# Optimization experiments

Hardware: AMD Instinct MI355X
Metric: run time of the kernel (lower is better)

The kernel has to match this reference:

```python
import jax, jax.numpy as jnp
import numpy as np

N = 50000      # nodes
E = 400000     # edges
D = 256        # args.dimensions
H1 = 32        # hidden1 (per-head)
HEADS = 4      # gat_heads
H2 = 64        # hidden2
DEC = 512      # decoder1
B = 4096       # number of entity index pairs
NEG = 0.2      # PyG GATConv leaky_relu negative slope


def setup_inputs() -> dict:
    key = jax.random.key(0)
    ks = jax.random.split(key, 24)
    s = lambda k, shape, fan: jax.random.normal(k, shape, jnp.float32) * (1.0 / np.sqrt(fan))
    return {
        "x_o": jax.random.normal(ks[0], (N, D), jnp.float32),
        "x_a": jax.random.normal(ks[1], (N, D), jnp.float32),
        "edge_index": jax.random.randint(ks[2], (2, E), 0, N, jnp.int32),
        "idx": jax.random.randint(ks[3], (2, B), 0, N, jnp.int32),
        # GATConv 1: in D -> H1 per head, HEADS heads, concat
        "W1": s(ks[4], (D, HEADS * H1), D),
        "a_src1": s(ks[5], (HEADS, H1), H1),
        "a_dst1": s(ks[6], (HEADS, H1), H1),
        "b1": jnp.zeros((HEADS * H1,), jnp.float32),
        "p1": jnp.full((HEADS * H1,), 0.25, jnp.float32),   # PReLU weight
        # GATConv 2: HEADS*H1 -> H2, 1 head, no concat
        "W2": s(ks[7], (HEADS * H1, H2), HEADS * H1),
        "a_src2": s(ks[8], (1, H2), H2),
        "a_dst2": s(ks[9], (1, H2), H2),
        "b2": jnp.zeros((H2,), jnp.float32),
        "p2": jnp.full((H2,), 0.25, jnp.float32),
        # mlp1
        "mlp_W": s(ks[10], (H2, H2), H2),
        "mlp_b": jnp.zeros((H2,), jnp.float32),
        # Discriminator bilinear (out=1)
        "disc_W": s(ks[11], (H2, H2), H2),
        "disc_b": jnp.zeros((), jnp.float32),
        # adversarial_logits linear (fixed, deterministic stand-in)
        "adv_W": s(ks[12], (H2, H2), H2),
        "adv_b": jnp.zeros((H2,), jnp.float32),
        # fusion decoder (stand-in for build_fusion_decoder): MLP with 2 heads
        "f_W1": s(ks[13], (2 * H2, DEC), 2 * H2),
        "f_b1": jnp.zeros((DEC,), jnp.float32),
        "f_W2": s(ks[14], (DEC, 2), DEC),
        "f_b2": jnp.zeros((2,), jnp.float32),
        "f_W3": s(ks[15], (DEC, 2), DEC),
        "f_b3": jnp.zeros((2,), jnp.float32),
    }


def prelu(x, w):
    return jnp.where(x >= 0, x, w * x)


def gat_conv(x, src, dst, W, a_src, a_dst, b, heads, out_dim, concat):
    # PyG GATConv (eval): per-head linear, edge attention, dst-segment softmax, scatter-sum.
    n = x.shape[0]
    h = (x @ W).reshape(n, heads, out_dim)                  # [N, H, F]
    a_s = (h * a_src[None]).sum(-1)                         # [N, H]
    a_d = (h * a_dst[None]).sum(-1)                         # [N, H]
    e = jax.nn.leaky_relu(a_s[src] + a_d[dst], NEG)         # [E', H]
    e_max = jax.ops.segment_max(e, dst, num_segments=n)
    w = jnp.exp(e - e_max[dst])
    denom = jax.ops.segment_sum(w, dst, num_segments=n)
    alpha = w / (denom[dst] + 1e-16)                        # [E', H]
    out = jax.ops.segment_sum(h[src] * alpha[..., None], dst, num_segments=n)  # [N, H, F]
    out = out.reshape(n, heads * out_dim) if concat else out.mean(1)
    return out + b


def encode(x, src, dst, W1, a_src1, a_dst1, b1, p1, W2, a_src2, a_dst2, b2, p2):
    x1 = prelu(gat_conv(x, src, dst, W1, a_src1, a_dst1, b1, HEADS, H1, True), p1)
    x2 = gat_conv(x1, src, dst, W2, a_src2, a_dst2, b2, 1, H2, False)
    return prelu(x2, p2)


def discriminate(c, h_pl, h_mi, disc_W, disc_b):
    # nn.Bilinear(n_h, n_h, 1) against broadcast summary c
    Wc = disc_W @ c                                          # [H2]
    sc_1 = h_pl @ Wc + disc_b                                # [N]
    sc_2 = h_mi @ Wc + disc_b                                # [N]
    return jnp.stack([sc_1, sc_2], axis=1)                   # [N, 2]


def reference(x_o, x_a, edge_index, idx,
              W1, a_src1, a_dst1, b1, p1,
              W2, a_src2, a_dst2, b2, p2,
              mlp_W, mlp_b, disc_W, disc_b, adv_W, adv_b,
              f_W1, f_b1, f_W2, f_b2, f_W3, f_b3):
    n = x_o.shape[0]
    loops = jnp.arange(n, dtype=edge_index.dtype)            # PyG add_self_loops=True
    src = jnp.concatenate([edge_index[0], loops])
    dst = jnp.concatenate([edge_index[1], loops])

    x2_o = encode(x_o, src, dst, W1, a_src1, a_dst1, b1, p1, W2, a_src2, a_dst2, b2, p2)
    x2_o_a = encode(x_a, src, dst, W1, a_src1, a_dst1, b1, p1, W2, a_src2, a_dst2, b2, p2)

    h_os = jax.nn.sigmoid(x2_o.mean(0)) @ mlp_W + mlp_b      # AvgReadout -> sigmoid -> mlp1
    h_os_a = jax.nn.sigmoid(x2_o_a.mean(0)) @ mlp_W + mlp_b

    ret_os = discriminate(h_os, x2_o, x2_o_a, disc_W, disc_b)
    ret_os_a = discriminate(h_os_a, x2_o_a, x2_o, disc_W, disc_b)

    # entities (task_type 'other' branch)
    e1 = x2_o[idx[0]]
    e2 = x2_o[idx[1]]
    fh = jax.nn.relu(jnp.concatenate([e1, e2], axis=-1) @ f_W1 + f_b1)
    log = fh @ f_W2 + f_b2
    log1 = fh @ f_W3 + f_b3

    sc_1 = (x2_o @ adv_W + adv_b).sum(1)[None, :]            # [1, N]
    sc_2 = (x2_o_a @ adv_W + adv_b).sum(1)[None, :]
    logits = jnp.concatenate([sc_1, sc_2], axis=1)           # [1, 2N]

    return (log, ret_os, ret_os_a, x2_o, logits, log1)
```

## Files before the change

### kernel.cpp

```cpp
#include <hip/hip_runtime.h>
#include <hip/hip_bf16.h>
#include <math.h>

constexpr int NN   = 50000;
constexpr int N2   = 2*NN;
constexpr int EE   = 400000;
constexpr int DIN  = 256;
constexpr int M1   = 128;
constexpr int H1N  = 4;
constexpr int M2   = 64;
constexpr int BP   = 4096;
constexpr int DEC  = 512;
constexpr float SLOPE = 0.2f;

constexpr int O_LOG    = 0;
constexpr int O_RETOS  = 8192;
constexpr int O_RETOSA = 108192;
constexpr int O_X2     = 208192;
constexpr int O_LOGITS = 3408192;
constexpr int O_LOG1   = 3508192;

constexpr int SCAN_NB = (NN + 1023) / 1024;

typedef __attribute__((ext_vector_type(8))) short short8;
typedef __attribute__((ext_vector_type(4))) float f32x4;

__device__ __forceinline__ short f2bs(float v){
    __hip_bfloat16 h = __float2bfloat16(v);
    unsigned short u; __builtin_memcpy(&u, &h, 2);
    return (short)u;
}
__device__ __forceinline__ float lrelu(float e){ return (e >= 0.f) ? e : SLOPE*e; }

__global__ void hist_dst(const int* __restrict__ edst, int* __restrict__ cnt){
    int i = blockIdx.x*blockDim.x + threadIdx.x;
    if (i < EE) atomicAdd(&cnt[edst[i]], 1);
}

__global__ __launch_bounds__(1024) void scan_blk(const int* __restrict__ cnt,
                                                 int* __restrict__ rowex,
                                                 int* __restrict__ bsum){
    __shared__ int wsum[16];
    const int t = threadIdx.x;
    const int idx = blockIdx.x*1024 + t;
    const int lane = t & 63, wid = t >> 6;
    int v = (idx < NN) ? cnt[idx] : 0;
    int s = v;
    #pragma unroll
    for (int o = 1; o < 64; o <<= 1){
        int u = __shfl_up(s, o, 64);
        if (lane >= o) s += u;
    }
    if (lane == 63) wsum[wid] = s;
    __syncthreads();
    if (wid == 0){
        int ws = (lane < 16) ? wsum[lane] : 0;
        #pragma unroll
        for (int o = 1; o < 16; o <<= 1){
            int u = __shfl_up(ws, o, 64);
            if (lane >= o) ws += u;
        }
        if (lane < 16) wsum[lane] = ws;
    }
    __syncthreads();
    int base = (wid > 0) ? wsum[wid-1] : 0;
    int incl = base + s;
    if (idx < NN) rowex[idx] = incl - v;
    if (t == 1023) bsum[blockIdx.x] = incl;
}

__global__ void scan_bsum(int* __restrict__ bsum, int nb){
    const int lane = threadIdx.x;
    int v = (lane < nb) ? bsum[lane] : 0;
    int s = v;
    #pragma unroll
    for (int o = 1; o < 64; o <<= 1){
        int u = __shfl_up(s, o, 64);
        if (lane >= o) s += u;
    }
    if (lane < nb) bsum[lane] = s - v;
}

__global__ void scan_fix(int* __restrict__ row, const int* __restrict__ bsum,
                         int* __restrict__ cursor){
    int idx = blockIdx.x*blockDim.x + threadIdx.x;
    if (idx < NN){
        int r = row[idx] + bsum[idx >> 10];
        row[idx] = r;
        cursor[idx] = r;
    }
    if (idx == 0) row[NN] = EE;
}

__global__ void fill_csr(const int* __restrict__ esrc, const int* __restrict__ edst,
                         int* __restrict__ cursor, int* __restrict__ adj){
    int i = blockIdx.x*blockDim.x + threadIdx.x;
    if (i >= EE) return;
    int d = edst[i];
    int slot = atomicAdd(&cursor[d], 1);
    adj[slot] = esrc[i];
}

__device__ __forceinline__ void pack_one(const float* __restrict__ W,
                                         __hip_bfloat16* __restrict__ Wpk,
                                         int i, int M){
    int k = i / M, c = i - k*M;
    int kb = k >> 5, r = k & 31, quad = r >> 3, j = r & 7;
    int ct = c >> 4, ln = quad*16 + (c & 15);
    int CT = M >> 4;
    size_t dst = (((size_t)kb*CT + ct)*64 + ln)*8 + j;
    Wpk[dst] = __float2bfloat16(W[i]);
}

__global__ void pack_all(const float* __restrict__ W1, const float* __restrict__ W2,
                         const float* __restrict__ fW1,
                         __hip_bfloat16* __restrict__ Wpk1,
                         __hip_bfloat16* __restrict__ Wpk2,
                         __hip_bfloat16* __restrict__ Wpkf){
    constexpr int S1 = DIN*M1;
    constexpr int S2 = S1 + M1*M2;
    constexpr int S3 = S2 + M1*DEC;
    int i = blockIdx.x*blockDim.x + threadIdx.x;
    if (i < S1)       pack_one(W1,  Wpk1, i,      M1);
    else if (i < S2)  pack_one(W2,  Wpk2, i - S1, M2);
    else if (i < S3)  pack_one(fW1, Wpkf, i - S2, DEC);
}

template<int K, int M, int HEADS_T, bool AF32>
__global__ __launch_bounds__(256) void gemm_attn(
        const void* __restrict__ X0, const void* __restrict__ X1,
        const __hip_bfloat16* __restrict__ Wpk,
        const float* __restrict__ asrc, const float* __restrict__ adst,
        __hip_bfloat16* __restrict__ Hb,
        float* __restrict__ AS, float* __restrict__ AD){
    constexpr int CT = M/16;
    constexpr int KB = K/32;
    constexpr int CPH = CT/HEADS_T;
    const int wave = (blockIdx.x*256 + threadIdx.x) >> 6;
    const int lane = threadIdx.x & 63;
    const int n0 = wave*16;
    if (n0 >= N2) return;
    const int arow = lane & 15;
    const int quad = lane >> 4;

    f32x4 acc[CT];
    #pragma unroll
    for (int ct = 0; ct < CT; ++ct) acc[ct] = (f32x4){0.f,0.f,0.f,0.f};

    const float* apf = nullptr;
    const __hip_bfloat16* apb = nullptr;
    if constexpr (AF32){
        apf = (n0 < NN) ? ((const float*)X0 + (size_t)(n0 + arow)*K)
                        : ((const float*)X1 + (size_t)(n0 - NN + arow)*K);
    } else {
        apb = (const __hip_bfloat16*)X0 + (size_t)(n0 + arow)*K;
    }

    for (int kb = 0; kb < KB; ++kb){
        const int kbase = kb*32 + quad*8;
        short8 af;
        if constexpr (AF32){
            float4 v0 = *(const float4*)(apf + kbase);
            float4 v1 = *(const float4*)(apf + kbase + 4);
            af[0]=f2bs(v0.x); af[1]=f2bs(v0.y); af[2]=f2bs(v0.z); af[3]=f2bs(v0.w);
            af[4]=f2bs(v1.x); af[5]=f2bs(v1.y); af[6]=f2bs(v1.z); af[7]=f2bs(v1.w);
        } else {
            af = *(const short8*)(apb + kbase);
        }
        const __hip_bfloat16* wp = Wpk + (size_t)kb*CT*64*8;
        #pragma unroll
        for (int ct = 0; ct < CT; ++ct){
            short8 bfr = *(const short8*)(wp + ((size_t)ct*64 + lane)*8);
            acc[ct] = __builtin_amdgcn_mfma_f32_16x16x32_bf16(af, bfr, acc[ct], 0, 0, 0);
        }
    }

    #pragma unroll
    for (int ct = 0; ct < CT; ++ct){
        #pragma unroll
        for (int r = 0; r < 4; ++r){
            int n = n0 + quad*4 + r;
            Hb[(size_t)n*M + ct*16 + arow] = __float2bfloat16(acc[ct][r]);
        }
    }

    float a_s[CT], a_d[CT];
    #pragma unroll
    for (int ct = 0; ct < CT; ++ct){
        a_s[ct] = asrc[ct*16 + arow];
        a_d[ct] = adst[ct*16 + arow];
    }
    #pragma unroll
    for (int r = 0; r < 4; ++r){
        const int n = n0 + quad*4 + r;
        #pragma unroll
        for (int h = 0; h < HEADS_T; ++h){
            float ss = 0.f, dd = 0.f;
            #pragma unroll
            for (int c2 = 0; c2 < CPH; ++c2){
                int ct = h*CPH + c2;
                ss += acc[ct][r]*a_s[ct];
                dd += acc[ct][r]*a_d[ct];
            }
            #pragma unroll
            for (int o = 8; o > 0; o >>= 1){
                ss += __shfl_down(ss, o, 16);
                dd += __shfl_down(dd, o, 16);
            }
            if (arow == 0){
                AS[(size_t)n*HEADS_T + h] = ss;
                AD[(size_t)n*HEADS_T + h] = dd;
            }
        }
    }
}

__global__ __launch_bounds__(256) void gat_agg_l1(
        const int* __restrict__ row, const int* __restrict__ adj,
        const __hip_bfloat16* __restrict__ Hfeat,
        const float* __restrict__ AS, const float* __restrict__ AD,
        const float* __restrict__ b, const float* __restrict__ p,
        __hip_bfloat16* __restrict__ outB){
    const int wv = (blockIdx.x*blockDim.x + threadIdx.x) >> 6;
    const int nw = (gridDim.x*blockDim.x) >> 6;
    const int t = threadIdx.x & 63;
    const int h = t >> 4;
    const unsigned* Hw = (const unsigned*)Hfeat;
    const float bb0 = b[2*t], bb1 = b[2*t+1];
    const float pp0 = p[2*t], pp1 = p[2*t+1];
    for (int nd = wv; nd < N2; nd += nw){
        const int g  = (nd < NN) ? nd : nd - NN;
        const int fb = nd - g;
        const float ad_h = AD[(size_t)nd*4 + h];
        float acc0, acc1, den;
        {
            float ws = __expf(lrelu(AS[(size_t)nd*4 + h] + ad_h));
            unsigned u = Hw[(size_t)nd*64 + t];
            acc0 = __uint_as_float(u << 16) * ws;
            acc1 = __uint_as_float(u & 0xffff0000u) * ws;
            den = ws;
        }
        const int beg = row[g], end = row[g+1];
        for (int j = beg; j < end; ++j){
            int s = adj[j] + fb;
            float wgt = __expf(lrelu(AS[(size_t)s*4 + h] + ad_h));
            unsigned u = Hw[(size_t)s*64 + t];
            acc0 += __uint_as_float(u << 16) * wgt;
            acc1 += __uint_as_float(u & 0xffff0000u) * wgt;
            den += wgt;
        }
        float inv = 1.f/(den + 1e-16f);
        float v0 = acc0*inv + bb0;
        float v1 = acc1*inv + bb1;
        v0 = (v0 >= 0.f) ? v0 : pp0*v0;
        v1 = (v1 >= 0.f) ? v1 : pp1*v1;
        ushort2 st = make_ushort2((unsigned short)f2bs(v0), (unsigned short)f2bs(v1));
        *(ushort2*)(outB + (size_t)nd*128 + 2*t) = st;
    }
}

__global__ __launch_bounds__(256) void gat_agg_l2(
        const int* __restrict__ row, const int* __restrict__ adj,
        const __hip_bfloat16* __restrict__ Hfeat,
        const float* __restrict__ AS, const float* __restrict__ AD,
        const float* __restrict__ b, const float* __restrict__ p,
        float* __restrict__ outO, float* __restrict__ outA){
    const int wv = (blockIdx.x*blockDim.x + threadIdx.x) >> 6;
    const int nw = (gridDim.x*blockDim.x) >> 6;
    const int t = threadIdx.x & 63;
    const float bb = b[t], pp = p[t];
    for (int nd = wv; nd < N2; nd += nw){
        const int g  = (nd < NN) ? nd : nd - NN;
        const int fb = nd - g;
        const float ad_d = AD[nd];
        float acc, den;
        {
            float ws = __expf(lrelu(AS[nd] + ad_d));
            acc = __bfloat162float(Hfeat[(size_t)nd*64 + t]) * ws;
            den = ws;
        }
        const int beg = row[g], end = row[g+1];
        for (int j = beg; j < end; ++j){
            int s = adj[j] + fb;
            float wgt = __expf(lrelu(AS[s] + ad_d));
            acc += __bfloat162float(Hfeat[(size_t)s*64 + t]) * wgt;
            den += wgt;
        }
        float v = acc/(den + 1e-16f) + bb;
        v = (v >= 0.f) ? v : pp*v;
        float* dst = (nd < NN) ? (outO + (size_t)nd*64) : (outA + (size_t)(nd - NN)*64);
        dst[t] = v;
    }
}

__global__ __launch_bounds__(256) void colsum2(const float* __restrict__ Xo,
                                               const float* __restrict__ Xa,
                                               float* __restrict__ outO,
                                               float* __restrict__ outA){
    __shared__ float red[2][256];
    const int t = threadIdx.x;
    const int c = t & 63;
    const int rg = t >> 6;
    float so = 0.f, sa = 0.f;
    for (int r = blockIdx.x*4 + rg; r < NN; r += gridDim.x*4){
        so += Xo[(size_t)r*64 + c];
        sa += Xa[(size_t)r*64 + c];
    }
    red[0][t] = so; red[1][t] = sa; __syncthreads();
    if (t < 64){
        atomicAdd(&outO[c], red[0][t] + red[0][t+64] + red[0][t+128] + red[0][t+192]);
        atomicAdd(&outA[c], red[1][t] + red[1][t+64] + red[1][t+128] + red[1][t+192]);
    }
}

__global__ void summary(const float* __restrict__ csum_o, const float* __restrict__ csum_a,
                        const float* __restrict__ mlpW, const float* __restrict__ mlpb,
                        const float* __restrict__ discW,
                        const float* __restrict__ advW, const float* __restrict__ advb,
                        float* __restrict__ Wc_o, float* __restrict__ Wc_a,
                        float* __restrict__ advRow, float* __restrict__ advbsum){
    __shared__ float s_o[64], s_a[64], h_o[64], h_a[64];
    const int t = threadIdx.x;
    s_o[t] = 1.f/(1.f + expf(-csum_o[t]/(float)NN));
    s_a[t] = 1.f/(1.f + expf(-csum_a[t]/(float)NN));
    __syncthreads();
    float ao = 0.f, aa = 0.f;
    for (int k = 0; k < 64; ++k){ float w = mlpW[k*64 + t]; ao += s_o[k]*w; aa += s_a[k]*w; }
    float bb = mlpb[t];
    h_o[t] = ao + bb; h_a[t] = aa + bb;
    __syncthreads();
    float wo = 0.f, wa = 0.f;
    for (int j = 0; j < 64; ++j){ float w = discW[t*64 + j]; wo += w*h_o[j]; wa += w*h_a[j]; }
    Wc_o[t] = wo; Wc_a[t] = wa;
    float ar = 0.f;
    for (int j = 0; j < 64; ++j) ar += advW[t*64 + j];
    advRow[t] = ar;
    float ab = advb[t];
    for (int o = 32; o > 0; o >>= 1) ab += __shfl_down(ab, o, 64);
    if (t == 0) advbsum[0] = ab;
}

__global__ void node_outputs(const float* __restrict__ x2o, const float* __restrict__ x2a,
                             const float* __restrict__ Wc_o, const float* __restrict__ Wc_a,
                             const float* __restrict__ advRow, const float* __restrict__ advbsum,
                             const float* __restrict__ discb,
                             float* __restrict__ out){
    const int n = blockIdx.x*4 + (threadIdx.x >> 6);
    const int l = threadIdx.x & 63;
    float xo = x2o[(size_t)n*64 + l], xa = x2a[(size_t)n*64 + l];
    float wo = Wc_o[l], wa = Wc_a[l], ar = advRow[l];
    float d1 = xo*wo, d2 = xa*wo, d3 = xa*wa, d4 = xo*wa, d5 = xo*ar, d6 = xa*ar;
    for (int o = 32; o > 0; o >>= 1){
        d1 += __shfl_down(d1, o, 64); d2 += __shfl_down(d2, o, 64);
        d3 += __shfl_down(d3, o, 64); d4 += __shfl_down(d4, o, 64);
        d5 += __shfl_down(d5, o, 64); d6 += __shfl_down(d6, o, 64);
    }
    if (l == 0){
        float db = discb[0];
        float ab = advbsum[0];
        out[O_RETOS  + n*2 + 0] = d1 + db;
        out[O_RETOS  + n*2 + 1] = d2 + db;
        out[O_RETOSA + n*2 + 0] = d3 + db;
        out[O_RETOSA + n*2 + 1] = d4 + db;
        out[O_LOGITS + n]       = d5 + ab;
        out[O_LOGITS + NN + n]  = d6 + ab;
    }
}

__global__ __launch_bounds__(256) void decoder_fused(
        const float* __restrict__ x2o, const int* __restrict__ idxArr,
        const __hip_bfloat16* __restrict__ Wpkf, const float* __restrict__ fb1,
        const float* __restrict__ fW2, const float* __restrict__ fb2,
        const float* __restrict__ fW3, const float* __restrict__ fb3,
        float* __restrict__ out){
    __shared__ float part[4][16][4];
    const int t = threadIdx.x;
    const int wid = t >> 6, lane = t & 63;
    const int arow = lane & 15, quad = lane >> 4;
    const int p0 = blockIdx.x*16;
    const int i0 = idxArr[p0 + arow];
    const int i1 = idxArr[BP + p0 + arow];

    f32x4 acc[8];
    #pragma unroll
    for (int c = 0; c < 8; ++c) acc[c] = (f32x4){0.f,0.f,0.f,0.f};

    #pragma unroll
    for (int kb = 0; kb < 4; ++kb){
        int src = (kb < 2) ? i0 : i1;
        int koff = (kb & 1)*32 + quad*8;
        const float* ap = x2o + (size_t)src*64 + koff;
        float4 v0 = *(const float4*)ap;
        float4 v1 = *(const float4*)(ap + 4);
        short8 af;
        af[0]=f2bs(v0.x); af[1]=f2bs(v0.y); af[2]=f2bs(v0.z); af[3]=f2bs(v0.w);
        af[4]=f2bs(v1.x); af[5]=f2bs(v1.y); af[6]=f2bs(v1.z); af[7]=f2bs(v1.w);
        const __hip_bfloat16* wp = Wpkf + (size_t)kb*32*64*8;
        #pragma unroll
        for (int c = 0; c < 8; ++c){
            int ct = wid*8 + c;
            short8 bfr = *(const short8*)(wp + ((size_t)ct*64 + lane)*8);
            acc[c] = __builtin_amdgcn_mfma_f32_16x16x32_bf16(af, bfr, acc[c], 0, 0, 0);
        }
    }

    float a0[4] = {0,0,0,0}, a1[4] = {0,0,0,0};
    float c0[4] = {0,0,0,0}, c1[4] = {0,0,0,0};
    #pragma unroll
    for (int c = 0; c < 8; ++c){
        int col = wid*128 + c*16 + arow;
        float bb = fb1[col];
        float w20 = fW2[col*2], w21 = fW2[col*2+1];
        float w30 = fW3[col*2], w31 = fW3[col*2+1];
        #pragma unroll
        for (int r = 0; r < 4; ++r){
            float v = acc[c][r] + bb;
            v = (v > 0.f) ? v : 0.f;
            a0[r] += v*w20; a1[r] += v*w21;
            c0[r] += v*w30; c1[r] += v*w31;
        }
    }
    #pragma unroll
    for (int o = 8; o > 0; o >>= 1){
        #pragma unroll
        for (int r = 0; r < 4; ++r){
            a0[r] += __shfl_down(a0[r], o, 16);
            a1[r] += __shfl_down(a1[r], o, 16);
            c0[r] += __shfl_down(c0[r], o, 16);
            c1[r] += __shfl_down(c1[r], o, 16);
        }
    }
    if (arow == 0){
        #pragma unroll
        for (int r = 0; r < 4; ++r){
            part[wid][quad*4 + r][0] = a0[r];
            part[wid][quad*4 + r][1] = a1[r];
            part[wid][quad*4 + r][2] = c0[r];
            part[wid][quad*4 + r][3] = c1[r];
        }
    }
    __syncthreads();
    if (t < 64){
        int pr = t >> 2, o = t & 3;
        float s = part[0][pr][o] + part[1][pr][o] + part[2][pr][o] + part[3][pr][o];
        int gb = p0 + pr;
        if (o == 0)      out[O_LOG  + gb*2 + 0] = s + fb2[0];
        else if (o == 1) out[O_LOG  + gb*2 + 1] = s + fb2[1];
        else if (o == 2) out[O_LOG1 + gb*2 + 0] = s + fb3[0];
        else             out[O_LOG1 + gb*2 + 1] = s + fb3[1];
    }
}

extern "C" void kernel_launch(void* const* d_in, const int* in_sizes, int n_in,
                              void* d_out, int out_size, void* d_ws, size_t ws_size,
                              hipStream_t stream){
    const float* x_o    = (const float*)d_in[0];
    const float* x_a    = (const float*)d_in[1];
    const int*   edge   = (const int*)d_in[2];
    const int*   idxp   = (const int*)d_in[3];
    const float* W1     = (const float*)d_in[4];
    const float* a_src1 = (const float*)d_in[5];
    const float* a_dst1 = (const float*)d_in[6];
    const float* b1     = (const float*)d_in[7];
    const float* p1     = (const float*)d_in[8];
    const float* W2     = (const float*)d_in[9];
    const float* a_src2 = (const float*)d_in[10];
    const float* a_dst2 = (const float*)d_in[11];
    const float* b2     = (const float*)d_in[12];
    const float* p2     = (const float*)d_in[13];
    const float* mlpW   = (const float*)d_in[14];
    const float* mlpb   = (const float*)d_in[15];
    const float* discW  = (const float*)d_in[16];
    const float* discb  = (const float*)d_in[17];
    const float* advW   = (const float*)d_in[18];
    const float* advb   = (const float*)d_in[19];
    const float* fW1    = (const float*)d_in[20];
    const float* fb1    = (const float*)d_in[21];
    const float* fW2    = (const float*)d_in[22];
    const float* fb2    = (const float*)d_in[23];
    const float* fW3    = (const float*)d_in[24];
    const float* fb3    = (const float*)d_in[25];

    const int* esrc = edge;
    const int* edst = edge + EE;

    float* w = (float*)d_ws;
    size_t off = 0;
    auto alloc = [&](size_t nfloats){ float* p = w + off; off += nfloats; return p; };
    __hip_bfloat16* Hb   = (__hip_bfloat16*)alloc((size_t)N2*M1/2);
    __hip_bfloat16* x1b  = (__hip_bfloat16*)alloc((size_t)N2*M1/2);
    float* asb   = alloc((size_t)N2*H1N);
    float* adb   = alloc((size_t)N2*H1N);
    __hip_bfloat16* Wpk1 = (__hip_bfloat16*)alloc((size_t)DIN*M1/2);
    __hip_bfloat16* Wpk2 = (__hip_bfloat16*)alloc((size_t)M1*M2/2);
    __hip_bfloat16* Wpkf = (__hip_bfloat16*)alloc((size_t)M1*DEC/2);
    int*   cnt   = (int*)alloc(NN);
    int*   row   = (int*)alloc(NN + 1);
    int*   cursor= (int*)alloc(NN);
    int*   adj   = (int*)alloc(EE);
    int*   bsum  = (int*)alloc(SCAN_NB + 1);
    float* smallb= alloc(512);
    float* csum_o = smallb;       float* csum_a = smallb + 64;
    float* Wc_o   = smallb + 128; float* Wc_a   = smallb + 192;
    float* advRow = smallb + 256; float* advbs  = smallb + 320;

    float* x2a = (float*)x1b;

    float* out = (float*)d_out;
    float* x2o = out + O_X2;

    hipMemsetAsync(cnt, 0, NN*sizeof(int), stream);
    hipMemsetAsync(smallb, 0, 128*sizeof(float), stream);
    hist_dst<<<(EE + 255)/256, 256, 0, stream>>>(edst, cnt);
    scan_blk<<<SCAN_NB, 1024, 0, stream>>>(cnt, row, bsum);
    scan_bsum<<<1, 64, 0, stream>>>(bsum, SCAN_NB);
    scan_fix<<<(NN + 255)/256, 256, 0, stream>>>(row, bsum, cursor);
    fill_csr<<<(EE + 255)/256, 256, 0, stream>>>(esrc, edst, cursor, adj);
    pack_all<<<(DIN*M1 + M1*M2 + M1*DEC + 255)/256, 256, 0, stream>>>(
        W1, W2, fW1, Wpk1, Wpk2, Wpkf);

    const int gw = ((N2/16) + 3) / 4;

    gemm_attn<DIN, M1, H1N, true><<<gw, 256, 0, stream>>>(
        x_o, x_a, Wpk1, a_src1, a_dst1, Hb, asb, adb);
    gat_agg_l1<<<2048, 256, 0, stream>>>(row, adj, Hb, asb, adb, b1, p1, x1b);

    gemm_attn<M1, M2, 1, false><<<gw, 256, 0, stream>>>(
        x1b, nullptr, Wpk2, a_src2, a_dst2, Hb, asb, adb);
    gat_agg_l2<<<2048, 256, 0, stream>>>(row, adj, Hb, asb, adb, b2, p2, x2o, x2a);

    colsum2<<<256, 256, 0, stream>>>(x2o, x2a, csum_o, csum_a);
    summary<<<1, 64, 0, stream>>>(csum_o, csum_a, mlpW, mlpb, discW, advW, advb,
                                  Wc_o, Wc_a, advRow, advbs);
    node_outputs<<<NN/4, 256, 0, stream>>>(x2o, x2a, Wc_o, Wc_a, advRow, advbs, discb, out);
    decoder_fused<<<BP/16, 256, 0, stream>>>(x2o, idxp, Wpkf, fb1, fW2, fb2, fW3, fb3, out);
}
```

Before: 493.3 us.

## Unroll GAT edge gathers by four and fuse column-sum into layer-2 aggregation

Both GAT aggregation kernels now handle neighbor edges four at a time, issuing the index, attention-score and feature loads together so more gather latency overlaps. The layer-2 aggregation also keeps a per-thread running column sum of its outputs and atomically adds it to the readout sums, which removes the separate colsum2 kernel that re-read both 50000x64 outputs. This adds one atomic per thread per wave (2048 blocks × 4 waves) on 64 addresses, and the unrolled loop uses more registers.

```diff
diff --git a/kernel.cpp b/kernel.cpp
--- a/kernel.cpp
+++ b/kernel.cpp
@@ -241,7 +241,35 @@
             den = ws;
         }
         const int beg = row[g], end = row[g+1];
-        for (int j = beg; j < end; ++j){
+        int j = beg;
+        for (; j + 3 < end; j += 4){
+            int s0 = adj[j]   + fb;
+            int s1 = adj[j+1] + fb;
+            int s2 = adj[j+2] + fb;
+            int s3 = adj[j+3] + fb;
+            float e0 = AS[(size_t)s0*4 + h];
+            float e1 = AS[(size_t)s1*4 + h];
+            float e2 = AS[(size_t)s2*4 + h];
+            float e3 = AS[(size_t)s3*4 + h];
+            unsigned u0 = Hw[(size_t)s0*64 + t];
+            unsigned u1 = Hw[(size_t)s1*64 + t];
+            unsigned u2 = Hw[(size_t)s2*64 + t];
+            unsigned u3 = Hw[(size_t)s3*64 + t];
+            float w0 = __expf(lrelu(e0 + ad_h));
+            float w1 = __expf(lrelu(e1 + ad_h));
+            float w2 = __expf(lrelu(e2 + ad_h));
+            float w3 = __expf(lrelu(e3 + ad_h));
+            acc0 += __uint_as_float(u0 << 16) * w0;
+            acc1 += __uint_as_float(u0 & 0xffff0000u) * w0;
+            acc0 += __uint_as_float(u1 << 16) * w1;
+            acc1 += __uint_as_float(u1 & 0xffff0000u) * w1;
+            acc0 += __uint_as_float(u2 << 16) * w2;
+            acc1 += __uint_as_float(u2 & 0xffff0000u) * w2;
+            acc0 += __uint_as_float(u3 << 16) * w3;
+            acc1 += __uint_as_float(u3 & 0xffff0000u) * w3;
+            den += w0 + w1 + w2 + w3;
+        }
+        for (; j < end; ++j){
             int s = adj[j] + fb;
             float wgt = __expf(lrelu(AS[(size_t)s*4 + h] + ad_h));
             unsigned u = Hw[(size_t)s*64 + t];
@@ -264,11 +292,14 @@
         const __hip_bfloat16* __restrict__ Hfeat,
         const float* __restrict__ AS, const float* __restrict__ AD,
         const float* __restrict__ b, const float* __restrict__ p,
-        float* __restrict__ outO, float* __restrict__ outA){
+        float* __restrict__ outO, float* __restrict__ outA,
+        float* __restrict__ csumO, float* __restrict__ csumA){
     const int wv = (blockIdx.x*blockDim.x + threadIdx.x) >> 6;
     const int nw = (gridDim.x*blockDim.x) >> 6;
     const int t = threadIdx.x & 63;
     const float bb = b[t], pp = p[t];
+    const ushort* Hu = (const ushort*)Hfeat;
+    float sO = 0.f, sA = 0.f;
     for (int nd = wv; nd < N2; nd += nw){
         const int g  = (nd < NN) ? nd : nd - NN;
         const int fb = nd - g;
@@ -276,41 +307,49 @@
         float acc, den;
         {
             float ws = __expf(lrelu(AS[nd] + ad_d));
-            acc = __bfloat162float(Hfeat[(size_t)nd*64 + t]) * ws;
+            unsigned u = Hu[(size_t)nd*64 + t];
+            acc = __uint_as_float(u << 16) * ws;
             den = ws;
         }
         const int beg = row[g], end = row[g+1];
-        for (int j = beg; j < end; ++j){
+        int j = beg;
+        for (; j + 3 < end; j += 4){
+            int s0 = adj[j]   + fb;
+            int s1 = adj[j+1] + fb;
+            int s2 = adj[j+2] + fb;
+            int s3 = adj[j+3] + fb;
+            float e0 = AS[s0];
+            float e1 = AS[s1];
+            float e2 = AS[s2];
+            float e3 = AS[s3];
+            unsigned u0 = Hu[(size_t)s0*64 + t];
+            unsigned u1 = Hu[(size_t)s1*64 + t];
+            unsigned u2 = Hu[(size_t)s2*64 + t];
+            unsigned u3 = Hu[(size_t)s3*64 + t];
+            float w0 = __expf(lrelu(e0 + ad_d));
+            float w1 = __expf(lrelu(e1 + ad_d));
+            float w2 = __expf(lrelu(e2 + ad_d));
+            float w3 = __expf(lrelu(e3 + ad_d));
+            acc += __uint_as_float(u0 << 16) * w0;
+            acc += __uint_as_float(u1 << 16) * w1;
+            acc += __uint_as_float(u2 << 16) * w2;
+            acc += __uint_as_float(u3 << 16) * w3;
+            den += w0 + w1 + w2 + w3;
+        }
+        for (; j < end; ++j){
             int s = adj[j] + fb;
             float wgt = __expf(lrelu(AS[s] + ad_d));
-            acc += __bfloat162float(Hfeat[(size_t)s*64 + t]) * wgt;
+            unsigned u = Hu[(size_t)s*64 + t];
+            acc += __uint_as_float(u << 16) * wgt;
             den += wgt;
         }
         float v = acc/(den + 1e-16f) + bb;
         v = (v >= 0.f) ? v : pp*v;
-        float* dst = (nd < NN) ? (outO + (size_t)nd*64) : (outA + (size_t)(nd - NN)*64);
-        dst[t] = v;
-    }
-}
-
-__global__ __launch_bounds__(256) void colsum2(const float* __restrict__ Xo,
-                                               const float* __restrict__ Xa,
-                                               float* __restrict__ outO,
-                                               float* __restrict__ outA){
-    __shared__ float red[2][256];
-    const int t = threadIdx.x;
-    const int c = t & 63;
-    const int rg = t >> 6;
-    float so = 0.f, sa = 0.f;
-    for (int r = blockIdx.x*4 + rg; r < NN; r += gridDim.x*4){
-        so += Xo[(size_t)r*64 + c];
-        sa += Xa[(size_t)r*64 + c];
-    }
-    red[0][t] = so; red[1][t] = sa; __syncthreads();
-    if (t < 64){
-        atomicAdd(&outO[c], red[0][t] + red[0][t+64] + red[0][t+128] + red[0][t+192]);
-        atomicAdd(&outA[c], red[1][t] + red[1][t+64] + red[1][t+128] + red[1][t+192]);
-    }
+        if (nd < NN){ outO[(size_t)nd*64 + t] = v; sO += v; }
+        else        { outA[(size_t)(nd - NN)*64 + t] = v; sA += v; }
+    }
+    atomicAdd(&csumO[t], sO);
+    atomicAdd(&csumA[t], sA);
 }
 
 __global__ void summary(const float* __restrict__ csum_o, const float* __restrict__ csum_a,
@@ -527,9 +566,9 @@
 
     gemm_attn<M1, M2, 1, false><<<gw, 256, 0, stream>>>(
         x1b, nullptr, Wpk2, a_src2, a_dst2, Hb, asb, adb);
-    gat_agg_l2<<<2048, 256, 0, stream>>>(row, adj, Hb, asb, adb, b2, p2, x2o, x2a);
-
-    colsum2<<<256, 256, 0, stream>>>(x2o, x2a, csum_o, csum_a);
+    gat_agg_l2<<<2048, 256, 0, stream>>>(row, adj, Hb, asb, adb, b2, p2,
+                                         x2o, x2a, csum_o, csum_a);
+
     summary<<<1, 64, 0, stream>>>(csum_o, csum_a, mlpW, mlpb, discW, advW, advb,
                                   Wc_o, Wc_a, advRow, advbs);
     node_outputs<<<NN/4, 256, 0, stream>>>(x2o, x2a, Wc_o, Wc_a, advRow, advbs, discb, out);
```

Result: slower. 646.7 us (+31.1%).
